# Kernel optimization log

Measured on AMD Instinct MI355X. Metric: run time of the kernel, lower is better.

Reference implementation:

```python
import jax, jax.numpy as jnp
import numpy as np

E, K, CAP = 6, 2, 192
ALPHA, LOAD_PEN, MIN_USE, TEMP = 0.7, 2.0, 0.05, 1.0
BN_EPS = 1e-5
NEG = -1e30


def conv3x3(x, w, b=None):
    y = jax.lax.conv_general_dilated(x, w, (1, 1), 'SAME',
                                     dimension_numbers=('NCHW', 'OIHW', 'NCHW'))
    if b is not None:
        y = y + b[None, :, None, None]
    return y


def bn_eval(x, g, b):
    # fresh BatchNorm buffers: running_mean=0, running_var=1
    s = g / jnp.sqrt(1.0 + BN_EPS)
    return x * s[None, :, None, None] + b[None, :, None, None]


def maxpool2(x):
    return jax.lax.reduce_window(x, -jnp.inf, jax.lax.max,
                                 (1, 1, 2, 2), (1, 1, 2, 2), 'VALID')


def avgpool_to2(x):
    B, C, H, W = x.shape
    return x.reshape(B, C, 2, H // 2, 2, W // 2).mean(axis=(3, 5))


def expert_forward(p, x):
    h = jax.nn.relu(bn_eval(conv3x3(x, p['c1w'], p['c1b']), p['b1g'], p['b1b']))
    h = maxpool2(h)  # 32 -> 16
    h = jax.nn.relu(bn_eval(conv3x3(h, p['c2w'], p['c2b']), p['b2g'], p['b2b']))
    h = jax.nn.relu(bn_eval(conv3x3(h, p['c3w'], p['c3b']), p['b3g'], p['b3b']))
    h = maxpool2(h)  # 16 -> 8
    h = jax.nn.relu(bn_eval(conv3x3(h, p['c4w'], p['c4b']), p['b4g'], p['b4b']))
    h = jax.nn.relu(bn_eval(conv3x3(h, p['c5w'], p['c5b']), p['b5g'], p['b5b']))
    feat = h.mean(axis=(2, 3))                       # global avg pool -> [B, c3]
    f = jax.nn.relu(feat @ p['fw'].T + p['fb'])      # [B, feat_dim]
    return f @ p['cw'].T + p['cb']                   # [B, num_classes]


def moe_forward(x, t_c1w, t_b1g, t_b1b, t_c2w, t_b2g, t_b2b, t_fcw, t_fcb,
                g1w, g1b, g2w, g2b,
                e_c1w, e_c1b, e_b1g, e_b1b, e_c2w, e_c2b, e_b2g, e_b2b,
                e_c3w, e_c3b, e_b3g, e_b3b, e_c4w, e_c4b, e_b4g, e_b4b,
                e_c5w, e_c5b, e_b5g, e_b5b, e_fw, e_fb, e_cw, e_cb, ema):
    B = x.shape[0]
    # --- routing trunk ---
    h = jax.nn.relu(bn_eval(conv3x3(x, t_c1w), t_b1g, t_b1b))
    h = jax.nn.relu(bn_eval(conv3x3(h, t_c2w), t_b2g, t_b2b))
    h = avgpool_to2(maxpool2(h)).reshape(B, -1)      # [B, 128]
    rf = jax.nn.relu(h @ t_fcw.T + t_fcb)            # [B, routing_dim]
    # --- gate (eval: no dropout, no noise) ---
    g = jax.nn.relu(rf @ g1w.T + g1b)
    gate_scores = (g @ g2w.T + g2b) / TEMP           # [B, E]
    # --- all experts on full batch (dense, as in source) ---
    ep = {'c1w': e_c1w, 'c1b': e_c1b, 'b1g': e_b1g, 'b1b': e_b1b,
          'c2w': e_c2w, 'c2b': e_c2b, 'b2g': e_b2g, 'b2b': e_b2b,
          'c3w': e_c3w, 'c3b': e_c3b, 'b3g': e_b3g, 'b3b': e_b3b,
          'c4w': e_c4w, 'c4b': e_c4b, 'b4g': e_b4g, 'b4b': e_b4b,
          'c5w': e_c5w, 'c5b': e_c5b, 'b5g': e_b5g, 'b5b': e_b5b,
          'fw': e_fw, 'fb': e_fb, 'cw': e_cw, 'cb': e_cb}
    logits_e = jax.vmap(expert_forward, in_axes=(0, None))(ep, x)  # [E, B, C]
    logits_e = jnp.transpose(logits_e, (1, 0, 2))                   # [B, E, C]
    # confidence = -entropy = sum p*log(p)
    logp = jax.nn.log_softmax(logits_e, axis=2)
    conf = (jnp.exp(logp) * jnp.log(jnp.exp(logp) + 1e-12)).sum(axis=2)  # [B, E]
    # --- balanced scores ---
    combined = ALPHA * gate_scores + (1.0 - ALPHA) * conf
    boost = jnp.where(ema < MIN_USE, (MIN_USE - ema) * 10.0, 0.0)
    combined = combined + boost[None, :]
    balanced = combined - LOAD_PEN * ema[None, :]
    # --- greedy capacity-constrained dispatch (deterministic order, eval) ---
    _, topk_idx = jax.lax.top_k(balanced, K)          # [B, K]

    def step(loads, idxs):
        l = loads[idxs]                                # [K]
        fits = l < CAP
        first = jnp.argmax(fits)                       # first expert with room
        fallback = idxs[jnp.argmin(l)]
        chosen = jnp.where(fits.any(), idxs[first], fallback)
        return loads.at[chosen].add(1.0), chosen

    _, chosen = jax.lax.scan(step, jnp.zeros((E,), balanced.dtype), topk_idx)
    D = jax.nn.one_hot(chosen, E, dtype=bool)          # [B, E]
    # --- weighted combine ---
    masked = jnp.where(D, balanced, NEG)
    w = jax.nn.softmax(masked, axis=1) * D.astype(balanced.dtype)
    w = w / (w.sum(axis=1, keepdims=True) + 1e-12)
    logits_final = (w[:, :, None] * logits_e).sum(axis=1)  # [B, C]
    return logits_final, balanced, D


def _params(key):
    ks = iter(jax.random.split(key, 64))
    rd, rd2, fd, nc, c1, c2, c3 = 64, 32, 128, 10, 32, 64, 128

    def w(shape, fan):
        return jax.random.normal(next(ks), shape, jnp.float32) * np.sqrt(2.0 / fan)

    p = {}
    p['t_c1w'] = w((32, 3, 3, 3), 32 * 9); p['t_b1g'] = jnp.ones(32); p['t_b1b'] = jnp.zeros(32)
    p['t_c2w'] = w((32, 32, 3, 3), 32 * 9); p['t_b2g'] = jnp.ones(32); p['t_b2b'] = jnp.zeros(32)
    p['t_fcw'] = w((rd, 128), rd); p['t_fcb'] = jnp.zeros(rd)
    p['g1w'] = w((rd2, rd), rd2); p['g1b'] = jnp.zeros(rd2)
    p['g2w'] = w((E, rd2), E); p['g2b'] = jnp.zeros(E)
    for i, (ci, co) in enumerate([(3, c1), (c1, c2), (c2, c2), (c2, c3), (c3, c3)], 1):
        p[f'e_c{i}w'] = w((E, co, ci, 3, 3), co * 9)
        p[f'e_c{i}b'] = jnp.zeros((E, co))
        p[f'e_b{i}g'] = jnp.ones((E, co))
        p[f'e_b{i}b'] = jnp.zeros((E, co))
    p['e_fw'] = w((E, fd, c3), fd); p['e_fb'] = jnp.zeros((E, fd))
    p['e_cw'] = w((E, nc, fd), nc); p['e_cb'] = jnp.zeros((E, nc))
    p['ema'] = jnp.ones((E,), jnp.float32) / E
    return p


def setup_inputs() -> dict:
    key = jax.random.key(0)
    kx, kp = jax.random.split(key)
    inp = {'x': jax.random.normal(kx, (1024, 3, 32, 32), jnp.float32)}
    inp.update(_params(kp))
    return inp


def reference(x, t_c1w, t_b1g, t_b1b, t_c2w, t_b2g, t_b2b, t_fcw, t_fcb,
              g1w, g1b, g2w, g2b,
              e_c1w, e_c1b, e_b1g, e_b1b, e_c2w, e_c2b, e_b2g, e_b2b,
              e_c3w, e_c3b, e_b3g, e_b3b, e_c4w, e_c4b, e_b4g, e_b4b,
              e_c5w, e_c5b, e_b5g, e_b5b, e_fw, e_fb, e_cw, e_cb, ema):
    return moe_forward(x, t_c1w, t_b1g, t_b1b, t_c2w, t_b2g, t_b2b, t_fcw, t_fcb,
                       g1w, g1b, g2w, g2b,
                       e_c1w, e_c1b, e_b1g, e_b1b, e_c2w, e_c2b, e_b2g, e_b2b,
                       e_c3w, e_c3b, e_b3g, e_b3b, e_c4w, e_c4b, e_b4g, e_b4b,
                       e_c5w, e_c5b, e_b5g, e_b5b, e_fw, e_fb, e_cw, e_cb, ema)
```

## Files before the change

kernel.cpp:

```cpp
#include <hip/hip_runtime.h>
#include <math.h>

#define B_ 1024
#define E_ 6

typedef _Float16 half8 __attribute__((ext_vector_type(8)));
typedef float f32x4 __attribute__((ext_vector_type(4)));

__device__ __forceinline__ unsigned short h_bits(_Float16 h) {
    union { _Float16 f; unsigned short u; } c; c.f = h; return c.u;
}
__device__ __forceinline__ unsigned int splitpack(float v) {
    _Float16 h = (_Float16)v;
    _Float16 l = (_Float16)((v - (float)h) * 2048.0f);
    return (unsigned int)h_bits(h) | ((unsigned int)h_bits(l) << 16);
}

__global__ void prep_w(const float* __restrict__ w, const float* __restrict__ g,
                       float* __restrict__ wout, int CO, int CI, int total) {
    int i = blockIdx.x * 256 + threadIdx.x;
    if (i >= total) return;
    int k = i % 9;
    int t = i / 9;
    int ci = t % CI; t /= CI;
    int co = t % CO;
    int e  = t / CO;
    float s = g[e * CO + co] * (1.0f / sqrtf(1.0f + 1e-5f));
    wout[(((long)(e * CI + ci) * 9 + k) * CO) + co] = w[i] * s;
}

__global__ void prep_b(const float* __restrict__ cb, const float* __restrict__ g,
                       const float* __restrict__ bb, float* __restrict__ bout, int N) {
    int i = blockIdx.x * 256 + threadIdx.x;
    if (i >= N) return;
    float s = g[i] * (1.0f / sqrtf(1.0f + 1e-5f));
    float c = (cb != nullptr) ? cb[i] : 0.0f;
    bout[i] = c * s + bb[i];
}

__global__ void prep_wfrag(const float* __restrict__ w, const float* __restrict__ g,
                           _Float16* __restrict__ out, int CI, int CO, int total) {
    int i = blockIdx.x * 256 + threadIdx.x;
    if (i >= total) return;
    const int NC = CI / 32;
    const int NB = CO / 16;
    int j = i & 7;
    int lane = (i >> 3) & 63;
    int rest = i >> 9;
    int chunk = rest % NC; rest /= NC;
    int tap = rest % 9; rest /= 9;
    int nbg = rest % NB;
    int e = rest / NB;
    int co = nbg * 16 + (lane & 15);
    int ci = chunk * 32 + ((lane >> 4) * 8) + j;
    float s = g[e * CO + co] * (1.0f / sqrtf(1.0f + 1e-5f));
    float v = w[(((long)(e * CO + co) * CI + ci) * 9) + tap] * s;
    _Float16 hi = (_Float16)v;
    _Float16 lo = (_Float16)((v - (float)hi) * 2048.0f);
    long perE = (long)NB * 9 * NC * 2 * 512;
    long F0 = ((long)(nbg * 9 + tap) * NC + chunk) * 2;
    long base = (long)e * perE + F0 * 512 + lane * 8 + j;
    out[base] = hi;
    out[base + 512] = lo;
}

template <int CI, int CO, int H, int TS, int CO_BLK, int CI_CHUNK, bool POOL, int OUTMODE>
__launch_bounds__(256)
__global__ void conv3x3(const float* __restrict__ in, const float* __restrict__ wt,
                        const float* __restrict__ bias, void* __restrict__ outv) {
    constexpr int TD = H / TS;
    constexpr int TILES = TD * TD;
    constexpr int LW = TS + 2;
    constexpr int NPX = POOL ? (TS / 2) * (TS / 2) : TS * TS;
    constexpr int G = 256 / NPX;
    constexpr int NG = CO / CO_BLK;
    constexpr int GPT = NG / G;
    constexpr int COT = GPT * CO_BLK;
    constexpr int NW = POOL ? 4 : 1;
    constexpr int OD = POOL ? TS / 2 : TS;

    __shared__ float lds[CI_CHUNK * LW * LW];

    int bid = blockIdx.x;
    int n = bid / TILES;
    int t = bid % TILES;
    int ty = (t / TD) * TS;
    int tx = (t % TD) * TS;
    int tid = threadIdx.x;
    int px = tid % NPX;
    int cg0 = tid / NPX;
    const int cg0s = __builtin_amdgcn_readfirstlane(cg0);
    int oy = px / OD;
    int ox = px % OD;

    float acc[NW][COT];
#pragma unroll
    for (int g2 = 0; g2 < GPT; ++g2)
#pragma unroll
        for (int j = 0; j < CO_BLK; ++j) {
            float bv = bias[(cg0s + g2 * G) * CO_BLK + j];
#pragma unroll
            for (int p = 0; p < NW; ++p) acc[p][g2 * CO_BLK + j] = bv;
        }

    for (int cc = 0; cc < CI / CI_CHUNK; ++cc) {
        const float* inb = in + ((long)n * CI + cc * CI_CHUNK) * (H * H);
        for (int idx = tid; idx < CI_CHUNK * LW * LW; idx += 256) {
            int ci = idx / (LW * LW);
            int r = idx - ci * (LW * LW);
            int yy = r / LW + ty - 1;
            int xx = r % LW + tx - 1;
            float v = 0.0f;
            if ((unsigned)yy < (unsigned)H && (unsigned)xx < (unsigned)H)
                v = inb[ci * H * H + yy * H + xx];
            lds[idx] = v;
        }
        __syncthreads();

        const float* wbase = wt + ((long)cc * CI_CHUNK) * 9 * CO;
        for (int ci = 0; ci < CI_CHUNK; ++ci) {
#pragma unroll
            for (int ky = 0; ky < 3; ++ky) {
#pragma unroll
                for (int kx = 0; kx < 3; ++kx) {
                    float v[NW];
                    if constexpr (POOL) {
#pragma unroll
                        for (int dy = 0; dy < 2; ++dy)
#pragma unroll
                            for (int dx = 0; dx < 2; ++dx)
                                v[dy * 2 + dx] =
                                    lds[ci * LW * LW + (2 * oy + dy + ky) * LW + (2 * ox + dx + kx)];
                    } else {
                        v[0] = lds[ci * LW * LW + (oy + ky) * LW + (ox + kx)];
                    }
                    const float* wr = wbase + ((ci * 3 + ky) * 3 + kx) * CO + cg0s * CO_BLK;
#pragma unroll
                    for (int g2 = 0; g2 < GPT; ++g2)
#pragma unroll
                        for (int j = 0; j < CO_BLK; ++j) {
                            float wv = wr[g2 * G * CO_BLK + j];
#pragma unroll
                            for (int p = 0; p < NW; ++p)
                                acc[p][g2 * CO_BLK + j] = fmaf(v[p], wv, acc[p][g2 * CO_BLK + j]);
                        }
                }
            }
        }
        __syncthreads();
    }

    if constexpr (OUTMODE == 1) {
        unsigned int* po = (unsigned int*)outv;
        long base;
        if constexpr (POOL) {
            constexpr int HP = H / 2;
            int pp = (ty / 2 + oy) * HP + (tx / 2 + ox);
            base = ((long)n * (HP * HP) + pp) * CO;
        } else {
            int pp = (ty + oy) * H + (tx + ox);
            base = ((long)n * (H * H) + pp) * CO;
        }
#pragma unroll
        for (int g2 = 0; g2 < GPT; ++g2) {
            int cobase = (cg0s + g2 * G) * CO_BLK;
#pragma unroll
            for (int j4 = 0; j4 < CO_BLK; j4 += 4) {
                uint4 u;
                unsigned int* up = (unsigned int*)&u;
#pragma unroll
                for (int jj = 0; jj < 4; ++jj) {
                    int a = g2 * CO_BLK + j4 + jj;
                    float v;
                    if constexpr (POOL)
                        v = fmaxf(fmaxf(acc[0][a], acc[1][a]), fmaxf(acc[2][a], acc[3][a]));
                    else
                        v = acc[0][a];
                    up[jj] = splitpack(fmaxf(v, 0.0f));
                }
                *(uint4*)(po + base + cobase + j4) = u;
            }
        }
    } else {
        float* out = (float*)outv;
        if constexpr (POOL) {
            constexpr int HP = H / 2;
            int py = ty / 2 + oy;
            int pxx = tx / 2 + ox;
#pragma unroll
            for (int g2 = 0; g2 < GPT; ++g2)
#pragma unroll
                for (int j = 0; j < CO_BLK; ++j) {
                    int co = (cg0s + g2 * G) * CO_BLK + j;
                    int a = g2 * CO_BLK + j;
                    float m = fmaxf(fmaxf(acc[0][a], acc[1][a]), fmaxf(acc[2][a], acc[3][a]));
                    out[((long)n * CO + co) * (HP * HP) + py * HP + pxx] = fmaxf(m, 0.0f);
                }
        } else {
            int yy = ty + oy;
            int xx = tx + ox;
#pragma unroll
            for (int g2 = 0; g2 < GPT; ++g2)
#pragma unroll
                for (int j = 0; j < CO_BLK; ++j) {
                    int co = (cg0s + g2 * G) * CO_BLK + j;
                    out[((long)n * CO + co) * (H * H) + yy * H + xx] =
                        fmaxf(acc[0][g2 * CO_BLK + j], 0.0f);
                }
        }
    }
}

__launch_bounds__(256, 2)
__global__ void conv_mfma_t2(const unsigned int* __restrict__ in,
                             const _Float16* __restrict__ wt,
                             const float* __restrict__ bias,
                             float* __restrict__ rf, int n0) {
    constexpr int PXS = 40;
    __shared__ _Float16 ldsH[18 * 18 * PXS];
    __shared__ _Float16 ldsL[18 * 18 * PXS];
    __shared__ float red[4][32];

    const int tid = threadIdx.x;
    const int wv = tid >> 6, lane = tid & 63;
    const int q = lane >> 4, l15 = lane & 15;
    const int bid = blockIdx.x;
    const int nl = bid >> 2, tile = bid & 3;
    const int ty2 = (tile >> 1) * 16, tx2 = (tile & 1) * 16;

    f32x4 accH[8], accL[8];
#pragma unroll
    for (int i = 0; i < 8; ++i) { accH[i] = (f32x4){0,0,0,0}; accL[i] = (f32x4){0,0,0,0}; }

    for (int u = tid; u < 18 * 18 * 8; u += 256) {
        int cu = u & 7;
        int p = u >> 3;
        int wy = p / 18, wx = p % 18;
        int gy = ty2 + wy - 1, gx = tx2 + wx - 1;
        uint4 w = make_uint4(0, 0, 0, 0);
        if ((unsigned)gy < 32u && (unsigned)gx < 32u)
            w = *(const uint4*)(in + ((long)nl * 1024 + gy * 32 + gx) * 32 + cu * 4);
        unsigned int h01 = (w.x & 0xffffu) | (w.y << 16);
        unsigned int h23 = (w.z & 0xffffu) | (w.w << 16);
        unsigned int l01 = (w.x >> 16) | (w.y & 0xffff0000u);
        unsigned int l23 = (w.z >> 16) | (w.w & 0xffff0000u);
        int fi = (wy * 18 + wx) * PXS + cu * 4;
        *(uint2*)(&ldsH[fi]) = make_uint2(h01, h23);
        *(uint2*)(&ldsL[fi]) = make_uint2(l01, l23);
    }
    __syncthreads();

#pragma unroll
    for (int ky = 0; ky < 3; ++ky)
#pragma unroll
        for (int kx = 0; kx < 3; ++kx) {
            const int tap = ky * 3 + kx;
            half8 ah[4], al[4];
#pragma unroll
            for (int mb = 0; mb < 4; ++mb) {
                int y = wv * 4 + mb;
                int fi = ((y + ky) * 18 + (l15 + kx)) * PXS + q * 8;
                ah[mb] = *(const half8*)&ldsH[fi];
                al[mb] = *(const half8*)&ldsL[fi];
            }
            half8 bh[2], bl[2];
#pragma unroll
            for (int nb = 0; nb < 2; ++nb) {
                int F0 = (nb * 9 + tap) * 2;
                bh[nb] = ((const half8*)wt)[(long)F0 * 64 + lane];
                bl[nb] = ((const half8*)wt)[(long)(F0 + 1) * 64 + lane];
            }
#pragma unroll
            for (int nb = 0; nb < 2; ++nb)
#pragma unroll
                for (int mb = 0; mb < 4; ++mb)
                    accH[mb * 2 + nb] = __builtin_amdgcn_mfma_f32_16x16x32_f16(
                        ah[mb], bh[nb], accH[mb * 2 + nb], 0, 0, 0);
#pragma unroll
            for (int nb = 0; nb < 2; ++nb)
#pragma unroll
                for (int mb = 0; mb < 4; ++mb)
                    accL[mb * 2 + nb] = __builtin_amdgcn_mfma_f32_16x16x32_f16(
                        ah[mb], bl[nb], accL[mb * 2 + nb], 0, 0, 0);
#pragma unroll
            for (int nb = 0; nb < 2; ++nb)
#pragma unroll
                for (int mb = 0; mb < 4; ++mb)
                    accL[mb * 2 + nb] = __builtin_amdgcn_mfma_f32_16x16x32_f16(
                        al[mb], bh[nb], accL[mb * 2 + nb], 0, 0, 0);
        }

    const float inv2048 = 1.0f / 2048.0f;
    float bv[2];
#pragma unroll
    for (int nb = 0; nb < 2; ++nb) bv[nb] = bias[nb * 16 + l15];
    float avg[2] = {0.0f, 0.0f};
#pragma unroll
    for (int k = 0; k < 2; ++k)
#pragma unroll
        for (int j = 0; j < 2; ++j)
#pragma unroll
            for (int nb = 0; nb < 2; ++nb) {
                float m = -1e30f;
#pragma unroll
                for (int dm = 0; dm < 2; ++dm)
#pragma unroll
                    for (int dr = 0; dr < 2; ++dr) {
                        int a = (2 * k + dm) * 2 + nb;
                        int r = 2 * j + dr;
                        float v = accH[a][r] + accL[a][r] * inv2048 + bv[nb];
                        m = fmaxf(m, v);
                    }
                avg[nb] += fmaxf(m, 0.0f);
            }
#pragma unroll
    for (int nb = 0; nb < 2; ++nb) {
        avg[nb] += __shfl_xor(avg[nb], 16);
        avg[nb] += __shfl_xor(avg[nb], 32);
    }
    if (q == 0) {
        red[wv][l15] = avg[0];
        red[wv][16 + l15] = avg[1];
    }
    __syncthreads();
    if (tid < 32) {
        float s = red[0][tid] + red[1][tid] + red[2][tid] + red[3][tid];
        int n = n0 + nl;
        rf[(long)n * 128 + tid * 4 + (tile >> 1) * 2 + (tile & 1)] = s * (1.0f / 64.0f);
    }
}

__launch_bounds__(512, 2)
__global__ void conv_expert(const float* __restrict__ x,
                            const float* __restrict__ w1, const float* __restrict__ b1,
                            const _Float16* __restrict__ wt2, const float* __restrict__ b2,
                            const _Float16* __restrict__ wt3, const float* __restrict__ b3,
                            const _Float16* __restrict__ wt4, const float* __restrict__ b4,
                            const _Float16* __restrict__ wt5, const float* __restrict__ b5,
                            float* __restrict__ feat) {
    __shared__ _Float16 pool[77760];
    _Float16* c2H = pool;
    _Float16* c2L = pool + 12960;
    _Float16* BH  = pool;
    _Float16* BL  = pool + 6400;
    float* xs  = (float*)(pool + 25920);
    float* w1s = (float*)(pool + 25920 + 6936);
    float* b1s = (float*)(pool + 25920 + 6936 + 1728);
    _Float16* AH = pool + 25920;
    _Float16* AL = pool + 51840;
    _Float16* CH = pool + 25920;
    _Float16* CL = pool + 38720;

    const int tid = threadIdx.x;
    const int wv = tid >> 6, lane = tid & 63;
    const int q = lane >> 4, l15 = lane & 15;
    const int rg = wv >> 1, ch2 = wv & 1;
    const int n = blockIdx.x;
    const float inv2048 = 1.0f / 2048.0f;

    {
        half8 z = {};
        half8* zp = (half8*)pool;
        for (int i = tid; i < 3240; i += 512) zp[i] = z;
    }
    for (int i = tid; i < 864; i += 512) w1s[i] = w1[i];
    if (tid < 32) b1s[tid] = b1[tid];
    for (int i = tid; i < 3 * 1156; i += 512) {
        int c = i / 1156;
        int r = i - c * 1156;
        int yy = r / 34 - 1, xx = r % 34 - 1;
        float v = 0.0f;
        if ((unsigned)yy < 32u && (unsigned)xx < 32u)
            v = x[((long)n * 3 + c) * 1024 + yy * 32 + xx];
        xs[i] = v;
    }
    __syncthreads();

    {
        const int pix = tid & 255;
        const int py1 = pix >> 4, px1 = pix & 15;
        const int coh = tid >> 8;
#pragma unroll
        for (int cg = 0; cg < 2; ++cg) {
            const int cog = coh * 2 + cg;
            float a[4][8];
#pragma unroll
            for (int j = 0; j < 8; ++j) {
                float bvv = b1s[cog * 8 + j];
#pragma unroll
                for (int p = 0; p < 4; ++p) a[p][j] = bvv;
            }
            for (int ci = 0; ci < 3; ++ci) {
                float patch[16];
#pragma unroll
                for (int r = 0; r < 4; ++r)
#pragma unroll
                    for (int cpx = 0; cpx < 4; ++cpx)
                        patch[r * 4 + cpx] = xs[ci * 1156 + (2 * py1 + r) * 34 + (2 * px1 + cpx)];
#pragma unroll
                for (int ky = 0; ky < 3; ++ky)
#pragma unroll
                    for (int kx = 0; kx < 3; ++kx) {
                        const float* wr = &w1s[((ci * 3 + ky) * 3 + kx) * 32 + cog * 8];
#pragma unroll
                        for (int j = 0; j < 8; ++j) {
                            float wvv = wr[j];
#pragma unroll
                            for (int dy = 0; dy < 2; ++dy)
#pragma unroll
                                for (int dx = 0; dx < 2; ++dx)
                                    a[dy * 2 + dx][j] =
                                        fmaf(patch[(dy + ky) * 4 + (dx + kx)], wvv,
                                             a[dy * 2 + dx][j]);
                        }
                    }
            }
            int fibase = ((py1 + 1) * 18 + (px1 + 1)) * 40 + cog * 8;
#pragma unroll
            for (int j = 0; j < 8; ++j) {
                float m = fmaxf(fmaxf(a[0][j], a[1][j]), fmaxf(a[2][j], a[3][j]));
                m = fmaxf(m, 0.0f);
                _Float16 hi = (_Float16)m;
                _Float16 lo = (_Float16)((m - (float)hi) * 2048.0f);
                c2H[fibase + j] = hi;
                c2L[fibase + j] = lo;
            }
        }
    }
    __syncthreads();

    for (int u = tid; u < 2 * 68 * 5; u += 512) {
        int g = u % 5;
        int t2 = u / 5;
        int ck = t2 / 68;
        int rp = t2 % 68;
        int wy, wx;
        if (rp < 18) { wy = 0; wx = rp; }
        else if (rp < 36) { wy = 17; wx = rp - 18; }
        else if (rp < 52) { wy = rp - 35; wx = 0; }
        else { wy = rp - 51; wx = 17; }
        int fi = ck * 12960 + (wy * 18 + wx) * 40 + g * 8;
        *(uint4*)(&AH[fi]) = make_uint4(0, 0, 0, 0);
        *(uint4*)(&AL[fi]) = make_uint4(0, 0, 0, 0);
    }

    f32x4 accH[8], accL[8];
#pragma unroll
    for (int i = 0; i < 8; ++i) { accH[i] = (f32x4){0,0,0,0}; accL[i] = (f32x4){0,0,0,0}; }

#pragma unroll
    for (int ky = 0; ky < 3; ++ky)
#pragma unroll
        for (int kx = 0; kx < 3; ++kx) {
            const int tap = ky * 3 + kx;
            half8 ah[4], al[4];
#pragma unroll
            for (int mb = 0; mb < 4; ++mb) {
                int y = rg * 4 + mb;
                int fi = ((y + ky) * 18 + (l15 + kx)) * 40 + q * 8;
                ah[mb] = *(const half8*)&c2H[fi];
                al[mb] = *(const half8*)&c2L[fi];
            }
            half8 bh[2], bl[2];
#pragma unroll
            for (int nb = 0; nb < 2; ++nb) {
                int nbg = ch2 * 2 + nb;
                int F0 = (nbg * 9 + tap) * 2;
                bh[nb] = ((const half8*)wt2)[(long)F0 * 64 + lane];
                bl[nb] = ((const half8*)wt2)[(long)(F0 + 1) * 64 + lane];
            }
#pragma unroll
            for (int nb = 0; nb < 2; ++nb)
#pragma unroll
                for (int mb = 0; mb < 4; ++mb)
                    accH[mb * 2 + nb] = __builtin_amdgcn_mfma_f32_16x16x32_f16(
                        ah[mb], bh[nb], accH[mb * 2 + nb], 0, 0, 0);
#pragma unroll
            for (int nb = 0; nb < 2; ++nb)
#pragma unroll
                for (int mb = 0; mb < 4; ++mb)
                    accL[mb * 2 + nb] = __builtin_amdgcn_mfma_f32_16x16x32_f16(
                        ah[mb], bl[nb], accL[mb * 2 + nb], 0, 0, 0);
#pragma unroll
            for (int nb = 0; nb < 2; ++nb)
#pragma unroll
                for (int mb = 0; mb < 4; ++mb)
                    accL[mb * 2 + nb] = __builtin_amdgcn_mfma_f32_16x16x32_f16(
                        al[mb], bh[nb], accL[mb * 2 + nb], 0, 0, 0);
        }
    {
        float bv[2];
#pragma unroll
        for (int nb = 0; nb < 2; ++nb) bv[nb] = b2[ch2 * 32 + nb * 16 + l15];
#pragma unroll
        for (int mb = 0; mb < 4; ++mb) {
            int y = rg * 4 + mb;
#pragma unroll
            for (int r = 0; r < 4; ++r) {
                int p = (y + 1) * 18 + (q * 4 + r + 1);
#pragma unroll
                for (int nb = 0; nb < 2; ++nb) {
                    float v = accH[mb * 2 + nb][r] + accL[mb * 2 + nb][r] * inv2048 + bv[nb];
                    v = fmaxf(v, 0.0f);
                    _Float16 hi = (_Float16)v;
                    _Float16 lo = (_Float16)((v - (float)hi) * 2048.0f);
                    int fi = ch2 * 12960 + p * 40 + nb * 16 + l15;
                    AH[fi] = hi;
                    AL[fi] = lo;
                }
            }
        }
    }
    __syncthreads();

#pragma unroll
    for (int i = 0; i < 8; ++i) { accH[i] = (f32x4){0,0,0,0}; accL[i] = (f32x4){0,0,0,0}; }

    for (int c = 0; c < 2; ++c) {
#pragma unroll
        for (int ky = 0; ky < 3; ++ky)
#pragma unroll
            for (int kx = 0; kx < 3; ++kx) {
                const int tap = ky * 3 + kx;
                half8 ah[4], al[4];
#pragma unroll
                for (int mb = 0; mb < 4; ++mb) {
                    int y = rg * 4 + mb;
                    int fi = c * 12960 + ((y + ky) * 18 + (l15 + kx)) * 40 + q * 8;
                    ah[mb] = *(const half8*)&AH[fi];
                    al[mb] = *(const half8*)&AL[fi];
                }
                half8 bh[2], bl[2];
#pragma unroll
                for (int nb = 0; nb < 2; ++nb) {
                    int nbg = ch2 * 2 + nb;
                    int F0 = ((nbg * 9 + tap) * 2 + c) * 2;
                    bh[nb] = ((const half8*)wt3)[(long)F0 * 64 + lane];
                    bl[nb] = ((const half8*)wt3)[(long)(F0 + 1) * 64 + lane];
                }
#pragma unroll
                for (int nb = 0; nb < 2; ++nb)
#pragma unroll
                    for (int mb = 0; mb < 4; ++mb)
                        accH[mb * 2 + nb] = __builtin_amdgcn_mfma_f32_16x16x32_f16(
                            ah[mb], bh[nb], accH[mb * 2 + nb], 0, 0, 0);
#pragma unroll
                for (int nb = 0; nb < 2; ++nb)
#pragma unroll
                    for (int mb = 0; mb < 4; ++mb)
                        accL[mb * 2 + nb] = __builtin_amdgcn_mfma_f32_16x16x32_f16(
                            ah[mb], bl[nb], accL[mb * 2 + nb], 0, 0, 0);
#pragma unroll
                for (int nb = 0; nb < 2; ++nb)
#pragma unroll
                    for (int mb = 0; mb < 4; ++mb)
                        accL[mb * 2 + nb] = __builtin_amdgcn_mfma_f32_16x16x32_f16(
                            al[mb], bh[nb], accL[mb * 2 + nb], 0, 0, 0);
            }
    }
    __syncthreads();

    for (int u = tid; u < 2 * 36 * 4; u += 512) {
        int g = u & 3;
        int t2 = u >> 2;
        int ck = t2 / 36;
        int rp = t2 % 36;
        int wy, wx;
        if (rp < 10) { wy = 0; wx = rp; }
        else if (rp < 20) { wy = 9; wx = rp - 10; }
        else if (rp < 28) { wy = rp - 19; wx = 0; }
        else { wy = rp - 27; wx = 9; }
        int fi = ck * 3200 + (wy * 10 + wx) * 32 + g * 8;
        *(uint4*)(&BH[fi]) = make_uint4(0, 0, 0, 0);
        *(uint4*)(&BL[fi]) = make_uint4(0, 0, 0, 0);
    }
    for (int u = tid; u < 4 * 36 * 4; u += 512) {
        int g = u & 3;
        int t2 = u >> 2;
        int ck = t2 / 36;
        int rp = t2 % 36;
        int wy, wx;
        if (rp < 10) { wy = 0; wx = rp; }
        else if (rp < 20) { wy = 9; wx = rp - 10; }
        else if (rp < 28) { wy = rp - 19; wx = 0; }
        else { wy = rp - 27; wx = 9; }
        int fi = ck * 3200 + (wy * 10 + wx) * 32 + g * 8;
        *(uint4*)(&CH[fi]) = make_uint4(0, 0, 0, 0);
        *(uint4*)(&CL[fi]) = make_uint4(0, 0, 0, 0);
    }
    {
        float bv[2];
#pragma unroll
        for (int nb = 0; nb < 2; ++nb) bv[nb] = b3[ch2 * 32 + nb * 16 + l15];
#pragma unroll
        for (int k = 0; k < 2; ++k)
#pragma unroll
            for (int j = 0; j < 2; ++j) {
                int yy = rg * 2 + k;
                int xx = q * 2 + j;
                int p = (yy + 1) * 10 + (xx + 1);
#pragma unroll
                for (int nb = 0; nb < 2; ++nb) {
                    float m = -1e30f;
#pragma unroll
                    for (int dm = 0; dm < 2; ++dm)
#pragma unroll
                        for (int dr = 0; dr < 2; ++dr) {
                            int a = (2 * k + dm) * 2 + nb;
                            int r = 2 * j + dr;
                            float v = accH[a][r] + accL[a][r] * inv2048 + bv[nb];
                            m = fmaxf(m, v);
                        }
                    m = fmaxf(m, 0.0f);
                    _Float16 hi = (_Float16)m;
                    _Float16 lo = (_Float16)((m - (float)hi) * 2048.0f);
                    int fi = ch2 * 3200 + p * 32 + nb * 16 + l15;
                    BH[fi] = hi;
                    BL[fi] = lo;
                }
            }
    }
    __syncthreads();

#pragma unroll
    for (int i = 0; i < 4; ++i) { accH[i] = (f32x4){0,0,0,0}; accL[i] = (f32x4){0,0,0,0}; }

    for (int c = 0; c < 2; ++c) {
#pragma unroll
        for (int ky = 0; ky < 3; ++ky)
#pragma unroll
            for (int kx = 0; kx < 3; ++kx) {
                const int tap = ky * 3 + kx;
                half8 ah[4], al[4];
#pragma unroll
                for (int mb = 0; mb < 4; ++mb) {
                    int m = mb * 16 + l15;
                    int p = ((m >> 3) + ky) * 10 + ((m & 7) + kx);
                    int fi = c * 3200 + p * 32 + q * 8;
                    ah[mb] = *(const half8*)&BH[fi];
                    al[mb] = *(const half8*)&BL[fi];
                }
                half8 bh, bl;
                {
                    int F0 = ((wv * 9 + tap) * 2 + c) * 2;
                    bh = ((const half8*)wt4)[(long)F0 * 64 + lane];
                    bl = ((const half8*)wt4)[(long)(F0 + 1) * 64 + lane];
                }
#pragma unroll
                for (int mb = 0; mb < 4; ++mb)
                    accH[mb] = __builtin_amdgcn_mfma_f32_16x16x32_f16(ah[mb], bh, accH[mb], 0, 0, 0);
#pragma unroll
                for (int mb = 0; mb < 4; ++mb)
                    accL[mb] = __builtin_amdgcn_mfma_f32_16x16x32_f16(ah[mb], bl, accL[mb], 0, 0, 0);
#pragma unroll
                for (int mb = 0; mb < 4; ++mb)
                    accL[mb] = __builtin_amdgcn_mfma_f32_16x16x32_f16(al[mb], bh, accL[mb], 0, 0, 0);
            }
    }
    {
        float bv = b4[wv * 16 + l15];
#pragma unroll
        for (int mb = 0; mb < 4; ++mb)
#pragma unroll
            for (int r = 0; r < 4; ++r) {
                int px = mb * 16 + q * 4 + r;
                int p = ((px >> 3) + 1) * 10 + ((px & 7) + 1);
                float v = accH[mb][r] + accL[mb][r] * inv2048 + bv;
                v = fmaxf(v, 0.0f);
                _Float16 hi = (_Float16)v;
                _Float16 lo = (_Float16)((v - (float)hi) * 2048.0f);
                int fi = (wv >> 1) * 3200 + p * 32 + (wv & 1) * 16 + l15;
                CH[fi] = hi;
                CL[fi] = lo;
            }
    }
    __syncthreads();

#pragma unroll
    for (int i = 0; i < 4; ++i) { accH[i] = (f32x4){0,0,0,0}; accL[i] = (f32x4){0,0,0,0}; }

    for (int c = 0; c < 4; ++c) {
#pragma unroll
        for (int ky = 0; ky < 3; ++ky)
#pragma unroll
            for (int kx = 0; kx < 3; ++kx) {
                const int tap = ky * 3 + kx;
                half8 ah[4], al[4];
#pragma unroll
                for (int mb = 0; mb < 4; ++mb) {
                    int m = mb * 16 + l15;
                    int p = ((m >> 3) + ky) * 10 + ((m & 7) + kx);
                    int fi = c * 3200 + p * 32 + q * 8;
                    ah[mb] = *(const half8*)&CH[fi];
                    al[mb] = *(const half8*)&CL[fi];
                }
                half8 bh, bl;
                {
                    int F0 = ((wv * 9 + tap) * 4 + c) * 2;
                    bh = ((const half8*)wt5)[(long)F0 * 64 + lane];
                    bl = ((const half8*)wt5)[(long)(F0 + 1) * 64 + lane];
                }
#pragma unroll
                for (int mb = 0; mb < 4; ++mb)
                    accH[mb] = __builtin_amdgcn_mfma_f32_16x16x32_f16(ah[mb], bh, accH[mb], 0, 0, 0);
#pragma unroll
                for (int mb = 0; mb < 4; ++mb)
                    accL[mb] = __builtin_amdgcn_mfma_f32_16x16x32_f16(ah[mb], bl, accL[mb], 0, 0, 0);
#pragma unroll
                for (int mb = 0; mb < 4; ++mb)
                    accL[mb] = __builtin_amdgcn_mfma_f32_16x16x32_f16(al[mb], bh, accL[mb], 0, 0, 0);
            }
    }
    {
        float bv = b5[wv * 16 + l15];
        float s = 0.0f;
#pragma unroll
        for (int mb = 0; mb < 4; ++mb)
#pragma unroll
            for (int r = 0; r < 4; ++r) {
                float v = accH[mb][r] + accL[mb][r] * inv2048 + bv;
                s += fmaxf(v, 0.0f);
            }
        s += __shfl_xor(s, 16);
        s += __shfl_xor(s, 32);
        if (lane < 16)
            feat[(long)n * 128 + wv * 16 + l15] = s * (1.0f / 64.0f);
    }
}

__launch_bounds__(128)
__global__ void head_k(const float* __restrict__ feat, const float* __restrict__ fw,
                       const float* __restrict__ fb, const float* __restrict__ cw,
                       const float* __restrict__ cb, float* __restrict__ outl) {
    __shared__ float fe[128];
    __shared__ float fv[128];
    int n = blockIdx.x, t = threadIdx.x;
    fe[t] = feat[(long)n * 128 + t];
    __syncthreads();
    const float* wr = fw + t * 128;
    float a = fb[t];
#pragma unroll 8
    for (int k = 0; k < 128; ++k) a = fmaf(fe[k], wr[k], a);
    fv[t] = fmaxf(a, 0.0f);
    __syncthreads();
    if (t < 10) {
        const float* cr = cw + t * 128;
        float a2 = cb[t];
#pragma unroll 8
        for (int k = 0; k < 128; ++k) a2 = fmaf(fv[k], cr[k], a2);
        outl[n * 10 + t] = a2;
    }
}

template <int I, int O, bool RELU>
__global__ void fc_k(const float* __restrict__ in, const float* __restrict__ W,
                     const float* __restrict__ bias, float* __restrict__ out) {
    int g = blockIdx.x * 256 + threadIdx.x;
    if (g >= B_ * O) return;
    int n = g / O;
    int o = g - n * O;
    const float* ip = in + (long)n * I;
    const float* wp = W + (long)o * I;
    float a = bias[o];
#pragma unroll 8
    for (int k = 0; k < I; ++k) a = fmaf(ip[k], wp[k], a);
    if (RELU) a = fmaxf(a, 0.0f);
    out[g] = a;
}

__global__ void conf_bal_k(const float* __restrict__ logitsE, const float* __restrict__ gate,
                           const float* __restrict__ ema, float* __restrict__ balanced,
                           unsigned char* __restrict__ cand) {
    int b = blockIdx.x * 256 + threadIdx.x;
    if (b >= B_) return;
    float bal[E_];
#pragma unroll
    for (int e = 0; e < E_; ++e) {
        const float* lp = logitsE + ((long)e * B_ + b) * 10;
        float m = lp[0];
#pragma unroll
        for (int k = 1; k < 10; ++k) m = fmaxf(m, lp[k]);
        float s = 0.0f;
#pragma unroll
        for (int k = 0; k < 10; ++k) s += expf(lp[k] - m);
        float ls = m + logf(s);
        float conf = 0.0f;
#pragma unroll
        for (int k = 0; k < 10; ++k) {
            float pp = expf(lp[k] - ls);
            conf += pp * logf(pp + 1e-12f);
        }
        float em = ema[e];
        float boost = (em < 0.05f) ? (0.05f - em) * 10.0f : 0.0f;
        bal[e] = 0.7f * gate[b * E_ + e] + 0.3f * conf + boost - 2.0f * em;
        balanced[b * E_ + e] = bal[e];
    }
    int i0 = 0;
    float m0 = bal[0];
#pragma unroll
    for (int e = 1; e < E_; ++e)
        if (bal[e] > m0) { m0 = bal[e]; i0 = e; }
    int i1 = -1;
    float m1 = -1e38f;
#pragma unroll
    for (int e = 0; e < E_; ++e)
        if (e != i0 && bal[e] > m1) { m1 = bal[e]; i1 = e; }
    cand[b] = (unsigned char)(i0 | (i1 << 3));
}

__global__ void dispatch_k(const unsigned char* __restrict__ cand, int* __restrict__ chosen) {
    int lane = threadIdx.x;
    unsigned long long L = 0;
    for (int r = 0; r < 16; ++r) {
        unsigned int v = cand[r * 64 + lane];
        int ch = 0;
        for (int q2 = 0; q2 < 64; ++q2) {
            unsigned int s = (unsigned int)__builtin_amdgcn_readlane((int)v, q2);
            unsigned int i0 = s & 7u;
            unsigned int i1 = (s >> 3) & 7u;
            unsigned int a0 = (unsigned int)(L >> (i0 * 10)) & 1023u;
            unsigned int a1 = (unsigned int)(L >> (i1 * 10)) & 1023u;
            unsigned int fb = (a1 < a0) ? i1 : i0;
            unsigned int c = (a0 < 192u) ? i0 : ((a1 < 192u) ? i1 : fb);
            if (lane == q2) ch = (int)c;
            L += 1ull << (c * 10);
        }
        chosen[r * 64 + lane] = ch;
    }
}

__global__ void final_k(const float* __restrict__ logitsE, const int* __restrict__ chosen,
                        float* __restrict__ out) {
    int b = blockIdx.x * 256 + threadIdx.x;
    if (b >= B_) return;
    int c = chosen[b];
    const float w = 1.0f / (1.0f + 1e-12f);
    const float* lp = logitsE + ((long)c * B_ + b) * 10;
#pragma unroll
    for (int k = 0; k < 10; ++k) out[b * 10 + k] = lp[k] * w;
    float* Dp = out + B_ * 10 + B_ * E_ + b * E_;
#pragma unroll
    for (int e = 0; e < E_; ++e) Dp[e] = (e == c) ? 1.0f : 0.0f;
}

extern "C" void kernel_launch(void* const* d_in, const int* in_sizes, int n_in,
                              void* d_out, int out_size, void* d_ws, size_t ws_size,
                              hipStream_t stream) {
    (void)in_sizes; (void)n_in; (void)out_size; (void)ws_size;
    const float* x     = (const float*)d_in[0];
    const float* t_c1w = (const float*)d_in[1];
    const float* t_b1g = (const float*)d_in[2];
    const float* t_b1b = (const float*)d_in[3];
    const float* t_c2w = (const float*)d_in[4];
    const float* t_b2g = (const float*)d_in[5];
    const float* t_b2b = (const float*)d_in[6];
    const float* t_fcw = (const float*)d_in[7];
    const float* t_fcb = (const float*)d_in[8];
    const float* g1w   = (const float*)d_in[9];
    const float* g1b   = (const float*)d_in[10];
    const float* g2w   = (const float*)d_in[11];
    const float* g2b   = (const float*)d_in[12];
    const float* e_c1w = (const float*)d_in[13];
    const float* e_c1b = (const float*)d_in[14];
    const float* e_b1g = (const float*)d_in[15];
    const float* e_b1b = (const float*)d_in[16];
    const float* e_c2w = (const float*)d_in[17];
    const float* e_c2b = (const float*)d_in[18];
    const float* e_b2g = (const float*)d_in[19];
    const float* e_b2b = (const float*)d_in[20];
    const float* e_c3w = (const float*)d_in[21];
    const float* e_c3b = (const float*)d_in[22];
    const float* e_b3g = (const float*)d_in[23];
    const float* e_b3b = (const float*)d_in[24];
    const float* e_c4w = (const float*)d_in[25];
    const float* e_c4b = (const float*)d_in[26];
    const float* e_b4g = (const float*)d_in[27];
    const float* e_b4b = (const float*)d_in[28];
    const float* e_c5w = (const float*)d_in[29];
    const float* e_c5b = (const float*)d_in[30];
    const float* e_b5g = (const float*)d_in[31];
    const float* e_b5b = (const float*)d_in[32];
    const float* e_fw  = (const float*)d_in[33];
    const float* e_fb  = (const float*)d_in[34];
    const float* e_cw  = (const float*)d_in[35];
    const float* e_cb  = (const float*)d_in[36];
    const float* ema   = (const float*)d_in[37];
    float* out = (float*)d_out;
    float* ws  = (float*)d_ws;

    size_t o = 0;
    float* R1f = ws + o; o += 8388608;
    float* R2f = ws + o; o += 16777216;
    float* rf_in   = ws + o; o += B_ * 128;
    float* rf      = ws + o; o += B_ * 64;
    float* gv      = ws + o; o += B_ * 32;
    float* gate    = ws + o; o += B_ * E_;
    float* logitsE = ws + o; o += E_ * B_ * 10;
    float* featb   = ws + o; o += B_ * 128;
    int*   chosen  = (int*)(ws + o); o += B_;
    unsigned char* cand = (unsigned char*)(ws + o); o += 256;
    float* wt_t1 = ws + o; o += 864;
    float* bt_t1 = ws + o; o += 32;
    float* bt_t2 = ws + o; o += 32;
    float* wt_c1 = ws + o; o += 6 * 864;
    float* bt_c1 = ws + o; o += 6 * 32;
    float* bt_c2 = ws + o; o += 6 * 64;
    float* bt_c3 = ws + o; o += 6 * 64;
    float* bt_c4 = ws + o; o += 6 * 128;
    float* bt_c5 = ws + o; o += 6 * 128;
    _Float16* wfrag_t2 = (_Float16*)(ws + o); o += 9216;
    _Float16* wfrag_c2 = (_Float16*)(ws + o); o += 110592;
    _Float16* wfrag_c3 = (_Float16*)(ws + o); o += 221184;
    _Float16* wfrag_c4 = (_Float16*)(ws + o); o += 442368;
    _Float16* wfrag_c5 = (_Float16*)(ws + o); o += 884736;

    unsigned int* R2u = (unsigned int*)R2f;
    (void)R1f;

    auto gsz = [](int n) { return (n + 255) / 256; };
    prep_w<<<gsz(864), 256, 0, stream>>>(t_c1w, t_b1g, wt_t1, 32, 3, 864);
    prep_b<<<1, 256, 0, stream>>>(nullptr, t_b1g, t_b1b, bt_t1, 32);
    prep_wfrag<<<gsz(9216), 256, 0, stream>>>(t_c2w, t_b2g, wfrag_t2, 32, 32, 9216);
    prep_b<<<1, 256, 0, stream>>>(nullptr, t_b2g, t_b2b, bt_t2, 32);
    prep_w<<<gsz(5184), 256, 0, stream>>>(e_c1w, e_b1g, wt_c1, 32, 3, 5184);
    prep_b<<<1, 256, 0, stream>>>(e_c1b, e_b1g, e_b1b, bt_c1, 192);
    prep_wfrag<<<gsz(110592), 256, 0, stream>>>(e_c2w, e_b2g, wfrag_c2, 32, 64, 110592);
    prep_b<<<2, 256, 0, stream>>>(e_c2b, e_b2g, e_b2b, bt_c2, 384);
    prep_wfrag<<<gsz(221184), 256, 0, stream>>>(e_c3w, e_b3g, wfrag_c3, 64, 64, 221184);
    prep_b<<<2, 256, 0, stream>>>(e_c3b, e_b3g, e_b3b, bt_c3, 384);
    prep_wfrag<<<gsz(442368), 256, 0, stream>>>(e_c4w, e_b4g, wfrag_c4, 64, 128, 442368);
    prep_b<<<3, 256, 0, stream>>>(e_c4b, e_b4g, e_b4b, bt_c4, 768);
    prep_wfrag<<<gsz(884736), 256, 0, stream>>>(e_c5w, e_b5g, wfrag_c5, 128, 128, 884736);
    prep_b<<<3, 256, 0, stream>>>(e_c5b, e_b5g, e_b5b, bt_c5, 768);

    for (int q = 0; q < 2; ++q) {
        const float* xq = x + (size_t)q * 512 * 3 * 1024;
        conv3x3<3, 32, 32, 16, 32, 3, false, 1><<<512 * 4, 256, 0, stream>>>(
            xq, wt_t1, bt_t1, (void*)R2u);
        conv_mfma_t2<<<512 * 4, 256, 0, stream>>>(R2u, wfrag_t2, bt_t2, rf_in, q * 512);
    }
    fc_k<128, 64, true><<<256, 256, 0, stream>>>(rf_in, t_fcw, t_fcb, rf);
    fc_k<64, 32, true><<<128, 256, 0, stream>>>(rf, g1w, g1b, gv);
    fc_k<32, 6, false><<<24, 256, 0, stream>>>(gv, g2w, g2b, gate);

    for (int e = 0; e < E_; ++e) {
        conv_expert<<<B_, 512, 0, stream>>>(
            x, wt_c1 + e * 864, bt_c1 + e * 32,
            wfrag_c2 + (size_t)e * 36864, bt_c2 + e * 64,
            wfrag_c3 + (size_t)e * 73728, bt_c3 + e * 64,
            wfrag_c4 + (size_t)e * 147456, bt_c4 + e * 128,
            wfrag_c5 + (size_t)e * 294912, bt_c5 + e * 128, featb);
        head_k<<<B_, 128, 0, stream>>>(featb, e_fw + e * 16384, e_fb + e * 128,
                                       e_cw + e * 1280, e_cb + e * 10,
                                       logitsE + (size_t)e * B_ * 10);
    }

    float* balanced = out + B_ * 10;
    conf_bal_k<<<4, 256, 0, stream>>>(logitsE, gate, ema, balanced, cand);
    dispatch_k<<<1, 64, 0, stream>>>(cand, chosen);
    final_k<<<4, 256, 0, stream>>>(logitsE, chosen, out);
}
```

Baseline: 1.323 ms.

## Batch all experts into single conv and head launches, pad LDS channel stride

The six per-expert launches of the conv and head kernels become one launch each over E*B blocks, with the expert index taken from the block index. The feature buffer grows to hold every expert's output. Separately, the per-pixel channel stride in the shared-memory tiles for conv4 and conv5 goes from 32 to 40 halves, which is meant to cut LDS bank conflicts on the half8 fragment loads. The merged launch drops the tail waves and gaps between launches but needs more workspace; the padded layout must still fit inside the existing shared pool.

```diff
diff --git a/kernel.cpp b/kernel.cpp
--- a/kernel.cpp
+++ b/kernel.cpp
@@ -332,31 +332,44 @@
 
 __launch_bounds__(512, 2)
 __global__ void conv_expert(const float* __restrict__ x,
-                            const float* __restrict__ w1, const float* __restrict__ b1,
-                            const _Float16* __restrict__ wt2, const float* __restrict__ b2,
-                            const _Float16* __restrict__ wt3, const float* __restrict__ b3,
-                            const _Float16* __restrict__ wt4, const float* __restrict__ b4,
-                            const _Float16* __restrict__ wt5, const float* __restrict__ b5,
-                            float* __restrict__ feat) {
+                            const float* __restrict__ w1b, const float* __restrict__ b1b_,
+                            const _Float16* __restrict__ wt2b, const float* __restrict__ b2b_,
+                            const _Float16* __restrict__ wt3b, const float* __restrict__ b3b_,
+                            const _Float16* __restrict__ wt4b, const float* __restrict__ b4b_,
+                            const _Float16* __restrict__ wt5b, const float* __restrict__ b5b_,
+                            float* __restrict__ featb) {
     __shared__ _Float16 pool[77760];
     _Float16* c2H = pool;
     _Float16* c2L = pool + 12960;
     _Float16* BH  = pool;
-    _Float16* BL  = pool + 6400;
+    _Float16* BL  = pool + 8000;
     float* xs  = (float*)(pool + 25920);
     float* w1s = (float*)(pool + 25920 + 6936);
     float* b1s = (float*)(pool + 25920 + 6936 + 1728);
     _Float16* AH = pool + 25920;
     _Float16* AL = pool + 51840;
     _Float16* CH = pool + 25920;
-    _Float16* CL = pool + 38720;
+    _Float16* CL = pool + 41920;
 
     const int tid = threadIdx.x;
     const int wv = tid >> 6, lane = tid & 63;
     const int q = lane >> 4, l15 = lane & 15;
     const int rg = wv >> 1, ch2 = wv & 1;
-    const int n = blockIdx.x;
+    const int e = blockIdx.x >> 10;
+    const int n = blockIdx.x & 1023;
     const float inv2048 = 1.0f / 2048.0f;
+
+    const float* w1 = w1b + e * 864;
+    const float* b1 = b1b_ + e * 32;
+    const _Float16* wt2 = wt2b + (size_t)e * 36864;
+    const float* b2 = b2b_ + e * 64;
+    const _Float16* wt3 = wt3b + (size_t)e * 73728;
+    const float* b3 = b3b_ + e * 64;
+    const _Float16* wt4 = wt4b + (size_t)e * 147456;
+    const float* b4 = b4b_ + e * 128;
+    const _Float16* wt5 = wt5b + (size_t)e * 294912;
+    const float* b5 = b5b_ + e * 128;
+    float* feat = featb + (size_t)e * (B_ * 128);
 
     {
         half8 z = {};
@@ -570,7 +583,7 @@
         else if (rp < 20) { wy = 9; wx = rp - 10; }
         else if (rp < 28) { wy = rp - 19; wx = 0; }
         else { wy = rp - 27; wx = 9; }
-        int fi = ck * 3200 + (wy * 10 + wx) * 32 + g * 8;
+        int fi = ck * 4000 + (wy * 10 + wx) * 40 + g * 8;
         *(uint4*)(&BH[fi]) = make_uint4(0, 0, 0, 0);
         *(uint4*)(&BL[fi]) = make_uint4(0, 0, 0, 0);
     }
@@ -584,7 +597,7 @@
         else if (rp < 20) { wy = 9; wx = rp - 10; }
         else if (rp < 28) { wy = rp - 19; wx = 0; }
         else { wy = rp - 27; wx = 9; }
-        int fi = ck * 3200 + (wy * 10 + wx) * 32 + g * 8;
+        int fi = ck * 4000 + (wy * 10 + wx) * 40 + g * 8;
         *(uint4*)(&CH[fi]) = make_uint4(0, 0, 0, 0);
         *(uint4*)(&CL[fi]) = make_uint4(0, 0, 0, 0);
     }
@@ -614,7 +627,7 @@
                     m = fmaxf(m, 0.0f);
                     _Float16 hi = (_Float16)m;
                     _Float16 lo = (_Float16)((m - (float)hi) * 2048.0f);
-                    int fi = ch2 * 3200 + p * 32 + nb * 16 + l15;
+                    int fi = ch2 * 4000 + p * 40 + nb * 16 + l15;
                     BH[fi] = hi;
                     BL[fi] = lo;
                 }
@@ -636,7 +649,7 @@
                 for (int mb = 0; mb < 4; ++mb) {
                     int m = mb * 16 + l15;
                     int p = ((m >> 3) + ky) * 10 + ((m & 7) + kx);
-                    int fi = c * 3200 + p * 32 + q * 8;
+                    int fi = c * 4000 + p * 40 + q * 8;
                     ah[mb] = *(const half8*)&BH[fi];
                     al[mb] = *(const half8*)&BL[fi];
                 }
@@ -669,7 +682,7 @@
                 v = fmaxf(v, 0.0f);
                 _Float16 hi = (_Float16)v;
                 _Float16 lo = (_Float16)((v - (float)hi) * 2048.0f);
-                int fi = (wv >> 1) * 3200 + p * 32 + (wv & 1) * 16 + l15;
+                int fi = (wv >> 1) * 4000 + p * 40 + (wv & 1) * 16 + l15;
                 CH[fi] = hi;
                 CL[fi] = lo;
             }
@@ -690,7 +703,7 @@
                 for (int mb = 0; mb < 4; ++mb) {
                     int m = mb * 16 + l15;
                     int p = ((m >> 3) + ky) * 10 + ((m & 7) + kx);
-                    int fi = c * 3200 + p * 32 + q * 8;
+                    int fi = c * 4000 + p * 40 + q * 8;
                     ah[mb] = *(const half8*)&CH[fi];
                     al[mb] = *(const half8*)&CL[fi];
                 }
@@ -729,12 +742,21 @@
 }
 
 __launch_bounds__(128)
-__global__ void head_k(const float* __restrict__ feat, const float* __restrict__ fw,
-                       const float* __restrict__ fb, const float* __restrict__ cw,
-                       const float* __restrict__ cb, float* __restrict__ outl) {
+__global__ void head_k(const float* __restrict__ featb, const float* __restrict__ fwb,
+                       const float* __restrict__ fbb, const float* __restrict__ cwb,
+                       const float* __restrict__ cbb, float* __restrict__ outlb) {
     __shared__ float fe[128];
     __shared__ float fv[128];
-    int n = blockIdx.x, t = threadIdx.x;
+    int e = blockIdx.x >> 10;
+    int n = blockIdx.x & 1023;
+    int t = threadIdx.x;
+    const float* feat = featb + (size_t)e * (B_ * 128);
+    const float* fw = fwb + (size_t)e * 16384;
+    const float* fb = fbb + e * 128;
+    const float* cw = cwb + (size_t)e * 1280;
+    const float* cb = cbb + e * 10;
+    float* outl = outlb + (size_t)e * (B_ * 10);
+
     fe[t] = feat[(long)n * 128 + t];
     __syncthreads();
     const float* wr = fw + t * 128;
@@ -896,7 +918,7 @@
     float* gv      = ws + o; o += B_ * 32;
     float* gate    = ws + o; o += B_ * E_;
     float* logitsE = ws + o; o += E_ * B_ * 10;
-    float* featb   = ws + o; o += B_ * 128;
+    float* featb   = ws + o; o += (size_t)E_ * B_ * 128;
     int*   chosen  = (int*)(ws + o); o += B_;
     unsigned char* cand = (unsigned char*)(ws + o); o += 256;
     float* wt_t1 = ws + o; o += 864;
@@ -943,17 +965,10 @@
     fc_k<64, 32, true><<<128, 256, 0, stream>>>(rf, g1w, g1b, gv);
     fc_k<32, 6, false><<<24, 256, 0, stream>>>(gv, g2w, g2b, gate);
 
-    for (int e = 0; e < E_; ++e) {
-        conv_expert<<<B_, 512, 0, stream>>>(
-            x, wt_c1 + e * 864, bt_c1 + e * 32,
-            wfrag_c2 + (size_t)e * 36864, bt_c2 + e * 64,
-            wfrag_c3 + (size_t)e * 73728, bt_c3 + e * 64,
-            wfrag_c4 + (size_t)e * 147456, bt_c4 + e * 128,
-            wfrag_c5 + (size_t)e * 294912, bt_c5 + e * 128, featb);
-        head_k<<<B_, 128, 0, stream>>>(featb, e_fw + e * 16384, e_fb + e * 128,
-                                       e_cw + e * 1280, e_cb + e * 10,
-                                       logitsE + (size_t)e * B_ * 10);
-    }
+    conv_expert<<<E_ * B_, 512, 0, stream>>>(
+        x, wt_c1, bt_c1, wfrag_c2, bt_c2, wfrag_c3, bt_c3,
+        wfrag_c4, bt_c4, wfrag_c5, bt_c5, featb);
+    head_k<<<E_ * B_, 128, 0, stream>>>(featb, e_fw, e_fb, e_cw, e_cb, logitsE);
 
     float* balanced = out + B_ * 10;
     conf_bal_k<<<4, 256, 0, stream>>>(logitsE, gate, ema, balanced, cand);
```

Result: no change. 1.325 ms (+0.1%).
